# Kernel tuning notes

Measured on AMD Instinct MI355X. Metric: run time of the kernel, lower is better.

## Reference

```python
import jax, jax.numpy as jnp
import numpy as np

EPS = 1e-5
N, K, CIN, COUT = 100000, 27, 64, 128


def sparse_conv(x, nbr, W):
    # x: [N, C]; nbr: [N, K] with sentinel index N meaning 'no neighbor'
    x_pad = jnp.concatenate([x, jnp.zeros((1, x.shape[1]), x.dtype)], axis=0)  # [N+1, C]
    g = x_pad[nbr]  # gather: [N, K, C]
    return jnp.einsum('nkc,kcd->nd', g, W)  # per-offset GEMM, scatter to output sites


def bn_relu(y, gamma, beta):
    # BatchNorm over active sites (training-mode batch statistics), then ReLU
    mu = y.mean(axis=0)
    var = y.var(axis=0)
    return jax.nn.relu((y - mu) * jax.lax.rsqrt(var + EPS) * gamma + beta)


def setup_inputs() -> dict:
    key = jax.random.key(0)
    ks = jax.random.split(key, 5)
    x = jax.random.normal(ks[0], (N, CIN), dtype=jnp.float32)
    # sentinel N indicates missing neighbor (maps to zero-padded row)
    nbr = jax.random.randint(ks[1], (N, K), 0, N + 1)
    W1 = jax.random.normal(ks[2], (K, CIN, COUT), dtype=jnp.float32) * (1.0 / np.sqrt(K * CIN))
    W2 = jax.random.normal(ks[3], (K, COUT, COUT), dtype=jnp.float32) * (1.0 / np.sqrt(K * COUT))
    W_skip = jax.random.normal(ks[4], (CIN, COUT), dtype=jnp.float32) * (1.0 / np.sqrt(CIN))
    return {
        'x': x, 'nbr': nbr,
        'W1': W1, 'gamma1': jnp.ones((COUT,), jnp.float32), 'beta1': jnp.zeros((COUT,), jnp.float32),
        'W2': W2, 'gamma2': jnp.ones((COUT,), jnp.float32), 'beta2': jnp.zeros((COUT,), jnp.float32),
        'W_skip': W_skip,
    }


def reference(x, nbr, W1, gamma1, beta1, W2, gamma2, beta2, W_skip):
    identity = x @ W_skip                      # 1x1 conv skip (same coords)
    h = bn_relu(sparse_conv(x, nbr, W1), gamma1, beta1)
    h = bn_relu(sparse_conv(h, nbr, W2), gamma2, beta2)
    return h + identity
```

## Files before the change

### kernel.cpp

```cpp
#include <hip/hip_runtime.h>
#include <hip/hip_bf16.h>

#define NSITES 100000
#define KOFFS 27
#define CIN 64
#define COUT 128

typedef unsigned short u16;
typedef __attribute__((ext_vector_type(8))) short s16x8;
typedef __attribute__((ext_vector_type(4))) float f32x4;

static __device__ __forceinline__ u16 f2bf(float f) {
    union { float f; unsigned u; } x; x.f = f;
    return (u16)((x.u + 0x7FFFu + ((x.u >> 16) & 1u)) >> 16);
}

__global__ void prep_kernel(const float* __restrict__ W1, const float* __restrict__ W2,
                            const float* __restrict__ Wsk,
                            u16* __restrict__ W1t, u16* __restrict__ W2t,
                            u16* __restrict__ Wskt, float* __restrict__ zero_area) {
    int i = blockIdx.x * 256 + threadIdx.x;
    if (i < 27 * 64 * 128) {
        int k = i / 8192, r = i & 8191, d = r >> 6, c = r & 63;
        W1t[i] = f2bf(W1[k * 8192 + c * 128 + d]);
        return;
    }
    i -= 27 * 64 * 128;
    if (i < 27 * 128 * 128) {
        int k = i / 16384, r = i & 16383, d = r >> 7, c = r & 127;
        W2t[i] = f2bf(W2[k * 16384 + c * 128 + d]);
        return;
    }
    i -= 27 * 128 * 128;
    if (i < 8192) {
        int d = i >> 6, c = i & 63;
        Wskt[i] = f2bf(Wsk[c * 128 + d]);
        return;
    }
    i -= 8192;
    zero_area[i] = 0.0f;
}

__global__ void convert_x_kernel(const float* __restrict__ x, u16* __restrict__ xb) {
    long long e = ((long long)blockIdx.x * 256 + threadIdx.x) * 8;
    if (e >= (long long)(NSITES + 1) * CIN) return;
    s16x8 o;
    if (e < (long long)NSITES * CIN) {
        float4 v0 = *(const float4*)(x + e);
        float4 v1 = *(const float4*)(x + e + 4);
        o[0] = (short)f2bf(v0.x); o[1] = (short)f2bf(v0.y);
        o[2] = (short)f2bf(v0.z); o[3] = (short)f2bf(v0.w);
        o[4] = (short)f2bf(v1.x); o[5] = (short)f2bf(v1.y);
        o[6] = (short)f2bf(v1.z); o[7] = (short)f2bf(v1.w);
    } else {
#pragma unroll
        for (int j = 0; j < 8; ++j) o[j] = 0;
    }
    *(s16x8*)(xb + e) = o;
}

template <int CK, bool IDENT, bool STATS>
__global__ __launch_bounds__(256, 3) void conv_kernel(
    const u16* __restrict__ xin, const int* __restrict__ nbr,
    const u16* __restrict__ Wt, float* __restrict__ yout,
    float* __restrict__ psum, float* __restrict__ psq, int nk) {
    constexpr int STRIDE = CK + 8;
    constexpr int KSTEPS = CK / 32;
    constexpr int CPR = CK / 8;
    constexpr int RPP = 256 / CPR;
    __shared__ __align__(16) u16 a_tile[64 * STRIDE];
    __shared__ int nbr_tile[IDENT ? 64 : 64 * KOFFS];

    const int tid = threadIdx.x;
    const int wave = tid >> 6;
    const int lane = tid & 63;
    const int m = lane & 15;
    const int q = lane >> 4;
    const int n0 = blockIdx.x * 64;
    const int wc = wave * 32;

    if (!IDENT) {
        for (int i = tid; i < 64 * KOFFS; i += 256) {
            int r = i / KOFFS;
            int kk = i - r * KOFFS;
            int row = n0 + r;
            nbr_tile[i] = (row < NSITES) ? nbr[row * KOFFS + kk] : NSITES;
        }
    }

    f32x4 acc[4][2];
#pragma unroll
    for (int rt = 0; rt < 4; ++rt)
#pragma unroll
        for (int ct = 0; ct < 2; ++ct)
#pragma unroll
            for (int r = 0; r < 4; ++r) acc[rt][ct][r] = 0.0f;

    const int srow = tid / CPR;
    const int schunk = tid % CPR;

    for (int k = 0; k < nk; ++k) {
        s16x8 bfrag[2][KSTEPS];
        const u16* wb = Wt + (long long)k * (COUT * CK);
#pragma unroll
        for (int ct = 0; ct < 2; ++ct)
#pragma unroll
            for (int ks = 0; ks < KSTEPS; ++ks) {
                int n = wc + ct * 16 + m;
                bfrag[ct][ks] = *(const s16x8*)(wb + n * CK + ks * 32 + q * 8);
            }

        __syncthreads();
#pragma unroll
        for (int p = 0; p < 64 / RPP; ++p) {
            int r = p * RPP + srow;
            int row = n0 + r;
            int idx;
            if (IDENT) idx = (row < NSITES) ? row : NSITES;
            else       idx = (row < NSITES) ? nbr_tile[r * KOFFS + k] : NSITES;
            s16x8 v = *(const s16x8*)(xin + (long long)idx * CK + schunk * 8);
            *(s16x8*)(a_tile + r * STRIDE + schunk * 8) = v;
        }
        __syncthreads();

#pragma unroll
        for (int ks = 0; ks < KSTEPS; ++ks) {
            s16x8 af[4];
#pragma unroll
            for (int rt = 0; rt < 4; ++rt)
                af[rt] = *(const s16x8*)(a_tile + (rt * 16 + m) * STRIDE + ks * 32 + q * 8);
#pragma unroll
            for (int rt = 0; rt < 4; ++rt)
#pragma unroll
                for (int ct = 0; ct < 2; ++ct)
                    acc[rt][ct] = __builtin_amdgcn_mfma_f32_16x16x32_bf16(
                        af[rt], bfrag[ct][ks], acc[rt][ct], 0, 0, 0);
        }
    }

#pragma unroll
    for (int rt = 0; rt < 4; ++rt) {
        int rowb = n0 + rt * 16 + q * 4;
#pragma unroll
        for (int ct = 0; ct < 2; ++ct) {
            int col = wc + ct * 16 + m;
#pragma unroll
            for (int r = 0; r < 4; ++r) {
                int row = rowb + r;
                if (row < NSITES) yout[(long long)row * COUT + col] = acc[rt][ct][r];
            }
        }
    }

    if (STATS) {
#pragma unroll
        for (int ct = 0; ct < 2; ++ct) {
            float s = 0.f, ss = 0.f;
#pragma unroll
            for (int rt = 0; rt < 4; ++rt)
#pragma unroll
                for (int r = 0; r < 4; ++r) {
                    float v = acc[rt][ct][r];
                    s += v; ss += v * v;
                }
            s += __shfl_xor(s, 16); ss += __shfl_xor(ss, 16);
            s += __shfl_xor(s, 32); ss += __shfl_xor(ss, 32);
            if (q == 0) {
                int col = wc + ct * 16 + m;
                int slot = blockIdx.x & 63;
                atomicAdd(psum + slot * COUT + col, s);
                atomicAdd(psq + slot * COUT + col, ss);
            }
        }
    }
}

__global__ void bn_stats_kernel(const float* __restrict__ psum, const float* __restrict__ psq,
                                const float* __restrict__ gamma, const float* __restrict__ beta,
                                float* __restrict__ ab) {
    int col = threadIdx.x;
    float s = 0.f, ss = 0.f;
    for (int i = 0; i < 64; ++i) { s += psum[i * COUT + col]; ss += psq[i * COUT + col]; }
    const float inv_n = 1.0f / (float)NSITES;
    float mu = s * inv_n;
    float var = ss * inv_n - mu * mu;
    float rs = rsqrtf(var + 1e-5f);
    float a = gamma[col] * rs;
    ab[col] = a;
    ab[COUT + col] = beta[col] - mu * a;
}

__global__ void bn_apply_kernel(const float* __restrict__ y, const float* __restrict__ ab,
                                u16* __restrict__ h) {
    long long e = ((long long)blockIdx.x * 256 + threadIdx.x) * 8;
    if (e >= (long long)(NSITES + 1) * COUT) return;
    s16x8 o;
    if (e < (long long)NSITES * COUT) {
        int cb = (int)(e & (COUT - 1));
        float4 v0 = *(const float4*)(y + e);
        float4 v1 = *(const float4*)(y + e + 4);
        float vs[8] = {v0.x, v0.y, v0.z, v0.w, v1.x, v1.y, v1.z, v1.w};
#pragma unroll
        for (int j = 0; j < 8; ++j) {
            float r = vs[j] * ab[cb + j] + ab[COUT + cb + j];
            o[j] = (short)f2bf(fmaxf(r, 0.f));
        }
    } else {
#pragma unroll
        for (int j = 0; j < 8; ++j) o[j] = 0;
    }
    *(s16x8*)(h + e) = o;
}

__global__ void final_kernel(const float* __restrict__ y, const float* __restrict__ ab,
                             float* __restrict__ out) {
    long long e = ((long long)blockIdx.x * 256 + threadIdx.x) * 8;
    if (e >= (long long)NSITES * COUT) return;
    int cb = (int)(e & (COUT - 1));
    float4 v0 = *(const float4*)(y + e);
    float4 v1 = *(const float4*)(y + e + 4);
    float4 i0 = *(const float4*)(out + e);
    float4 i1 = *(const float4*)(out + e + 4);
    float vs[8] = {v0.x, v0.y, v0.z, v0.w, v1.x, v1.y, v1.z, v1.w};
    float is[8] = {i0.x, i0.y, i0.z, i0.w, i1.x, i1.y, i1.z, i1.w};
    float os[8];
#pragma unroll
    for (int j = 0; j < 8; ++j) {
        float r = vs[j] * ab[cb + j] + ab[COUT + cb + j];
        os[j] = fmaxf(r, 0.f) + is[j];
    }
    *(float4*)(out + e) = make_float4(os[0], os[1], os[2], os[3]);
    *(float4*)(out + e + 4) = make_float4(os[4], os[5], os[6], os[7]);
}

extern "C" void kernel_launch(void* const* d_in, const int* in_sizes, int n_in,
                              void* d_out, int out_size, void* d_ws, size_t ws_size,
                              hipStream_t stream) {
    const float* x   = (const float*)d_in[0];
    const int*   nbr = (const int*)d_in[1];
    const float* W1  = (const float*)d_in[2];
    const float* g1  = (const float*)d_in[3];
    const float* b1  = (const float*)d_in[4];
    const float* W2  = (const float*)d_in[5];
    const float* g2  = (const float*)d_in[6];
    const float* b2  = (const float*)d_in[7];
    const float* Wsk = (const float*)d_in[8];
    float* out = (float*)d_out;

    char* ws = (char*)d_ws;
    u16*   xb   = (u16*)(ws);
    u16*   W1t  = (u16*)(ws + 12800128);
    u16*   W2t  = (u16*)(ws + 13242496);
    u16*   Wskt = (u16*)(ws + 14127232);
    float* y    = (float*)(ws + 14143616);
    u16*   h1   = (u16*)(ws + 65343616);
    float* ps1  = (float*)(ws + 90943872);
    float* pq1  = ps1 + 8192;
    float* ps2  = pq1 + 8192;
    float* pq2  = ps2 + 8192;
    float* ab1  = pq2 + 8192;
    float* ab2  = ab1 + 256;

    const int NBLK = (NSITES + 63) / 64;

    prep_kernel<<<2752, 256, 0, stream>>>(W1, W2, Wsk, W1t, W2t, Wskt, ps1);
    convert_x_kernel<<<3126, 256, 0, stream>>>(x, xb);
    conv_kernel<64, true, false><<<NBLK, 256, 0, stream>>>(xb, nullptr, Wskt, out, nullptr, nullptr, 1);
    conv_kernel<64, false, true><<<NBLK, 256, 0, stream>>>(xb, nbr, W1t, y, ps1, pq1, KOFFS);
    bn_stats_kernel<<<1, 128, 0, stream>>>(ps1, pq1, g1, b1, ab1);
    bn_apply_kernel<<<6251, 256, 0, stream>>>(y, ab1, h1);
    conv_kernel<128, false, true><<<NBLK, 256, 0, stream>>>(h1, nbr, W2t, y, ps2, pq2, KOFFS);
    bn_stats_kernel<<<1, 128, 0, stream>>>(ps2, pq2, g2, b2, ab2);
    final_kernel<<<6250, 256, 0, stream>>>(y, ab2, out);
}
```

Before: 514.3 us.

## Prefetch neighbor gathers two offsets ahead, fuse skip GEMM, store conv output as bf16

The conv loop now holds gathered input rows for the next two offsets in registers, so global gather latency overlaps with the MFMA work on the current offset. The 1x1 skip GEMM is folded into the first conv kernel's epilogue, which removes one launch and one pass over x. The intermediate conv outputs are stored in bf16 instead of fp32, halving that write/read traffic. The trade-offs are higher register pressure from the prefetch buffers, an extra sync per iteration, and BN statistics still taken from fp32 accumulators while normalization is applied to bf16-rounded values.

```diff
diff --git a/kernel.cpp b/kernel.cpp
--- a/kernel.cpp
+++ b/kernel.cpp
@@ -13,6 +13,10 @@
 static __device__ __forceinline__ u16 f2bf(float f) {
     union { float f; unsigned u; } x; x.f = f;
     return (u16)((x.u + 0x7FFFu + ((x.u >> 16) & 1u)) >> 16);
+}
+static __device__ __forceinline__ float bf2f(u16 v) {
+    union { unsigned u; float f; } x; x.u = ((unsigned)v) << 16;
+    return x.f;
 }
 
 __global__ void prep_kernel(const float* __restrict__ W1, const float* __restrict__ W2,
@@ -59,17 +63,19 @@
     *(s16x8*)(xb + e) = o;
 }
 
-template <int CK, bool IDENT, bool STATS>
+template <int CK, bool IDENT_FUSE, bool STATS>
 __global__ __launch_bounds__(256, 3) void conv_kernel(
     const u16* __restrict__ xin, const int* __restrict__ nbr,
-    const u16* __restrict__ Wt, float* __restrict__ yout,
-    float* __restrict__ psum, float* __restrict__ psq, int nk) {
+    const u16* __restrict__ Wt, u16* __restrict__ yout,
+    float* __restrict__ psum, float* __restrict__ psq, int nk,
+    const u16* __restrict__ Wskt, float* __restrict__ outid) {
     constexpr int STRIDE = CK + 8;
     constexpr int KSTEPS = CK / 32;
     constexpr int CPR = CK / 8;
     constexpr int RPP = 256 / CPR;
+    constexpr int NPASS = 64 / RPP;
     __shared__ __align__(16) u16 a_tile[64 * STRIDE];
-    __shared__ int nbr_tile[IDENT ? 64 : 64 * KOFFS];
+    __shared__ int nbr_tile[64 * KOFFS];
 
     const int tid = threadIdx.x;
     const int wave = tid >> 6;
@@ -78,48 +84,58 @@
     const int q = lane >> 4;
     const int n0 = blockIdx.x * 64;
     const int wc = wave * 32;
-
-    if (!IDENT) {
-        for (int i = tid; i < 64 * KOFFS; i += 256) {
-            int r = i / KOFFS;
-            int kk = i - r * KOFFS;
-            int row = n0 + r;
-            nbr_tile[i] = (row < NSITES) ? nbr[row * KOFFS + kk] : NSITES;
-        }
-    }
-
-    f32x4 acc[4][2];
-#pragma unroll
-    for (int rt = 0; rt < 4; ++rt)
-#pragma unroll
-        for (int ct = 0; ct < 2; ++ct)
-#pragma unroll
-            for (int r = 0; r < 4; ++r) acc[rt][ct][r] = 0.0f;
-
     const int srow = tid / CPR;
     const int schunk = tid % CPR;
 
-    for (int k = 0; k < nk; ++k) {
-        s16x8 bfrag[2][KSTEPS];
+    for (int i = tid; i < 64 * KOFFS; i += 256) {
+        int r = i / KOFFS;
+        int kk = i - r * KOFFS;
+        int row = n0 + r;
+        nbr_tile[i] = (row < NSITES) ? nbr[row * KOFFS + kk] : NSITES;
+    }
+    __syncthreads();
+
+    f32x4 acc[4][2];
+#pragma unroll
+    for (int rt = 0; rt < 4; ++rt)
+#pragma unroll
+        for (int ct = 0; ct < 2; ++ct)
+#pragma unroll
+            for (int r = 0; r < 4; ++r) acc[rt][ct][r] = 0.0f;
+
+    s16x8 ag0[NPASS], ag1[NPASS];
+#pragma unroll
+    for (int p = 0; p < NPASS; ++p) {
+        int r = p * RPP + srow;
+        ag0[p] = *(const s16x8*)(xin + (long long)nbr_tile[r * KOFFS] * CK + schunk * 8);
+    }
+    if (nk > 1) {
+#pragma unroll
+        for (int p = 0; p < NPASS; ++p) {
+            int r = p * RPP + srow;
+            ag1[p] = *(const s16x8*)(xin + (long long)nbr_tile[r * KOFFS + 1] * CK + schunk * 8);
+        }
+    }
+
+    auto conv_iter = [&](int k, s16x8 (&agc)[NPASS]) {
+        s16x8 bf[2][KSTEPS];
         const u16* wb = Wt + (long long)k * (COUT * CK);
 #pragma unroll
         for (int ct = 0; ct < 2; ++ct)
 #pragma unroll
-            for (int ks = 0; ks < KSTEPS; ++ks) {
-                int n = wc + ct * 16 + m;
-                bfrag[ct][ks] = *(const s16x8*)(wb + n * CK + ks * 32 + q * 8);
+            for (int ks = 0; ks < KSTEPS; ++ks)
+                bf[ct][ks] = *(const s16x8*)(wb + (wc + ct * 16 + m) * CK + ks * 32 + q * 8);
+
+#pragma unroll
+        for (int p = 0; p < NPASS; ++p)
+            *(s16x8*)(a_tile + (p * RPP + srow) * STRIDE + schunk * 8) = agc[p];
+
+        if (k + 2 < nk) {
+#pragma unroll
+            for (int p = 0; p < NPASS; ++p) {
+                int r = p * RPP + srow;
+                agc[p] = *(const s16x8*)(xin + (long long)nbr_tile[r * KOFFS + k + 2] * CK + schunk * 8);
             }
-
-        __syncthreads();
-#pragma unroll
-        for (int p = 0; p < 64 / RPP; ++p) {
-            int r = p * RPP + srow;
-            int row = n0 + r;
-            int idx;
-            if (IDENT) idx = (row < NSITES) ? row : NSITES;
-            else       idx = (row < NSITES) ? nbr_tile[r * KOFFS + k] : NSITES;
-            s16x8 v = *(const s16x8*)(xin + (long long)idx * CK + schunk * 8);
-            *(s16x8*)(a_tile + r * STRIDE + schunk * 8) = v;
         }
         __syncthreads();
 
@@ -134,8 +150,14 @@
 #pragma unroll
                 for (int ct = 0; ct < 2; ++ct)
                     acc[rt][ct] = __builtin_amdgcn_mfma_f32_16x16x32_bf16(
-                        af[rt], bfrag[ct][ks], acc[rt][ct], 0, 0, 0);
-        }
+                        af[rt], bf[ct][ks], acc[rt][ct], 0, 0, 0);
+        }
+        __syncthreads();
+    };
+
+    for (int k = 0; k < nk; k += 2) {
+        conv_iter(k, ag0);
+        if (k + 1 < nk) conv_iter(k + 1, ag1);
     }
 
 #pragma unroll
@@ -147,7 +169,7 @@
 #pragma unroll
             for (int r = 0; r < 4; ++r) {
                 int row = rowb + r;
-                if (row < NSITES) yout[(long long)row * COUT + col] = acc[rt][ct][r];
+                if (row < NSITES) yout[(long long)row * COUT + col] = f2bf(acc[rt][ct][r]);
             }
         }
     }
@@ -170,6 +192,58 @@
                 int slot = blockIdx.x & 63;
                 atomicAdd(psum + slot * COUT + col, s);
                 atomicAdd(psq + slot * COUT + col, ss);
+            }
+        }
+    }
+
+    if (IDENT_FUSE) {
+#pragma unroll
+        for (int rt = 0; rt < 4; ++rt)
+#pragma unroll
+            for (int ct = 0; ct < 2; ++ct)
+#pragma unroll
+                for (int r = 0; r < 4; ++r) acc[rt][ct][r] = 0.0f;
+        s16x8 aid[NPASS];
+#pragma unroll
+        for (int p = 0; p < NPASS; ++p) {
+            int row = n0 + p * RPP + srow;
+            long long idx = (row < NSITES) ? row : NSITES;
+            aid[p] = *(const s16x8*)(xin + idx * CK + schunk * 8);
+        }
+        s16x8 bfi[2][KSTEPS];
+#pragma unroll
+        for (int ct = 0; ct < 2; ++ct)
+#pragma unroll
+            for (int ks = 0; ks < KSTEPS; ++ks)
+                bfi[ct][ks] = *(const s16x8*)(Wskt + (wc + ct * 16 + m) * CK + ks * 32 + q * 8);
+#pragma unroll
+        for (int p = 0; p < NPASS; ++p)
+            *(s16x8*)(a_tile + (p * RPP + srow) * STRIDE + schunk * 8) = aid[p];
+        __syncthreads();
+#pragma unroll
+        for (int ks = 0; ks < KSTEPS; ++ks) {
+            s16x8 af[4];
+#pragma unroll
+            for (int rt = 0; rt < 4; ++rt)
+                af[rt] = *(const s16x8*)(a_tile + (rt * 16 + m) * STRIDE + ks * 32 + q * 8);
+#pragma unroll
+            for (int rt = 0; rt < 4; ++rt)
+#pragma unroll
+                for (int ct = 0; ct < 2; ++ct)
+                    acc[rt][ct] = __builtin_amdgcn_mfma_f32_16x16x32_bf16(
+                        af[rt], bfi[ct][ks], acc[rt][ct], 0, 0, 0);
+        }
+#pragma unroll
+        for (int rt = 0; rt < 4; ++rt) {
+            int rowb = n0 + rt * 16 + q * 4;
+#pragma unroll
+            for (int ct = 0; ct < 2; ++ct) {
+                int col = wc + ct * 16 + m;
+#pragma unroll
+                for (int r = 0; r < 4; ++r) {
+                    int row = rowb + r;
+                    if (row < NSITES) outid[(long long)row * COUT + col] = acc[rt][ct][r];
+                }
             }
         }
     }
@@ -190,19 +264,17 @@
     ab[COUT + col] = beta[col] - mu * a;
 }
 
-__global__ void bn_apply_kernel(const float* __restrict__ y, const float* __restrict__ ab,
+__global__ void bn_apply_kernel(const u16* __restrict__ y, const float* __restrict__ ab,
                                 u16* __restrict__ h) {
     long long e = ((long long)blockIdx.x * 256 + threadIdx.x) * 8;
     if (e >= (long long)(NSITES + 1) * COUT) return;
     s16x8 o;
     if (e < (long long)NSITES * COUT) {
         int cb = (int)(e & (COUT - 1));
-        float4 v0 = *(const float4*)(y + e);
-        float4 v1 = *(const float4*)(y + e + 4);
-        float vs[8] = {v0.x, v0.y, v0.z, v0.w, v1.x, v1.y, v1.z, v1.w};
+        s16x8 v = *(const s16x8*)(y + e);
 #pragma unroll
         for (int j = 0; j < 8; ++j) {
-            float r = vs[j] * ab[cb + j] + ab[COUT + cb + j];
+            float r = bf2f((u16)v[j]) * ab[cb + j] + ab[COUT + cb + j];
             o[j] = (short)f2bf(fmaxf(r, 0.f));
         }
     } else {
@@ -212,21 +284,19 @@
     *(s16x8*)(h + e) = o;
 }
 
-__global__ void final_kernel(const float* __restrict__ y, const float* __restrict__ ab,
+__global__ void final_kernel(const u16* __restrict__ y, const float* __restrict__ ab,
                              float* __restrict__ out) {
     long long e = ((long long)blockIdx.x * 256 + threadIdx.x) * 8;
     if (e >= (long long)NSITES * COUT) return;
     int cb = (int)(e & (COUT - 1));
-    float4 v0 = *(const float4*)(y + e);
-    float4 v1 = *(const float4*)(y + e + 4);
+    s16x8 v = *(const s16x8*)(y + e);
     float4 i0 = *(const float4*)(out + e);
     float4 i1 = *(const float4*)(out + e + 4);
-    float vs[8] = {v0.x, v0.y, v0.z, v0.w, v1.x, v1.y, v1.z, v1.w};
     float is[8] = {i0.x, i0.y, i0.z, i0.w, i1.x, i1.y, i1.z, i1.w};
     float os[8];
 #pragma unroll
     for (int j = 0; j < 8; ++j) {
-        float r = vs[j] * ab[cb + j] + ab[COUT + cb + j];
+        float r = bf2f((u16)v[j]) * ab[cb + j] + ab[COUT + cb + j];
         os[j] = fmaxf(r, 0.f) + is[j];
     }
     *(float4*)(out + e) = make_float4(os[0], os[1], os[2], os[3]);
@@ -252,9 +322,9 @@
     u16*   W1t  = (u16*)(ws + 12800128);
     u16*   W2t  = (u16*)(ws + 13242496);
     u16*   Wskt = (u16*)(ws + 14127232);
-    float* y    = (float*)(ws + 14143616);
-    u16*   h1   = (u16*)(ws + 65343616);
-    float* ps1  = (float*)(ws + 90943872);
+    u16*   y    = (u16*)(ws + 14143616);
+    u16*   h1   = (u16*)(ws + 39743616);
+    float* ps1  = (float*)(ws + 65343872);
     float* pq1  = ps1 + 8192;
     float* ps2  = pq1 + 8192;
     float* pq2  = ps2 + 8192;
@@ -265,11 +335,10 @@
 
     prep_kernel<<<2752, 256, 0, stream>>>(W1, W2, Wsk, W1t, W2t, Wskt, ps1);
     convert_x_kernel<<<3126, 256, 0, stream>>>(x, xb);
-    conv_kernel<64, true, false><<<NBLK, 256, 0, stream>>>(xb, nullptr, Wskt, out, nullptr, nullptr, 1);
-    conv_kernel<64, false, true><<<NBLK, 256, 0, stream>>>(xb, nbr, W1t, y, ps1, pq1, KOFFS);
+    conv_kernel<64, true, true><<<NBLK, 256, 0, stream>>>(xb, nbr, W1t, y, ps1, pq1, KOFFS, Wskt, out);
     bn_stats_kernel<<<1, 128, 0, stream>>>(ps1, pq1, g1, b1, ab1);
     bn_apply_kernel<<<6251, 256, 0, stream>>>(y, ab1, h1);
-    conv_kernel<128, false, true><<<NBLK, 256, 0, stream>>>(h1, nbr, W2t, y, ps2, pq2, KOFFS);
+    conv_kernel<128, false, true><<<NBLK, 256, 0, stream>>>(h1, nbr, W2t, y, ps2, pq2, KOFFS, nullptr, nullptr);
     bn_stats_kernel<<<1, 128, 0, stream>>>(ps2, pq2, g2, b2, ab2);
     final_kernel<<<6250, 256, 0, stream>>>(y, ab2, out);
 }
```

New measurement: 456.1 us. -11.3%, faster.
